# Performance work log

Hardware: AMD Instinct MI355X
Metric: run time of the kernel (lower is better)

Reference implementation:

```python
import jax, jax.numpy as jnp
import numpy as np

N_NODES = 50000
N_EDGES = 800000
IN_C = 32
HID = 64
N_LAYERS = 3
EDGE_HID = 128
OUT_C = 1
N_GRAPHS = 8


def setup_inputs() -> dict:
    key = jax.random.key(0)
    ks = jax.random.split(key, 32)
    x = jax.random.normal(ks[0], (N_NODES, IN_C), dtype=jnp.float32)
    # edges with src != dst so that PyG's remove_self_loops is a no-op
    src = jax.random.randint(ks[1], (N_EDGES,), 0, N_NODES)
    off = jax.random.randint(ks[2], (N_EDGES,), 1, N_NODES)
    dst = (src + off) % N_NODES
    edge_index = jnp.stack([src, dst]).astype(jnp.int32)
    batch = jnp.sort(jax.random.randint(ks[3], (N_NODES,), 0, N_GRAPHS)).astype(jnp.int32)
    inp = {"x": x, "edge_index": edge_index, "batch": batch}
    i = 4
    for l in range(N_LAYERS):
        din = IN_C if l == 0 else HID
        s = 1.0 / float(np.sqrt(din))
        inp[f"Wl{l}"] = jax.random.normal(ks[i], (din, HID), dtype=jnp.float32) * s; i += 1
        inp[f"bl{l}"] = jnp.zeros((HID,), jnp.float32)
        inp[f"Wr{l}"] = jax.random.normal(ks[i], (din, HID), dtype=jnp.float32) * s; i += 1
        inp[f"br{l}"] = jnp.zeros((HID,), jnp.float32)
        inp[f"att{l}"] = jax.random.normal(ks[i], (HID,), dtype=jnp.float32) * (1.0 / float(np.sqrt(HID))); i += 1
        inp[f"res{l}"] = jax.random.normal(ks[i], (din, HID), dtype=jnp.float32) * s; i += 1
        inp[f"bias{l}"] = jnp.zeros((HID,), jnp.float32)
        inp[f"lng{l}"] = jnp.ones((HID,), jnp.float32)
        inp[f"lnb{l}"] = jnp.zeros((HID,), jnp.float32)
    efd = 3 * HID
    inp["W1"] = jax.random.normal(ks[i], (efd, EDGE_HID), dtype=jnp.float32) * (1.0 / float(np.sqrt(efd))); i += 1
    inp["b1"] = jnp.zeros((EDGE_HID,), jnp.float32)
    inp["W2"] = jax.random.normal(ks[i], (EDGE_HID, OUT_C), dtype=jnp.float32) * (1.0 / float(np.sqrt(EDGE_HID))); i += 1
    inp["b2"] = jnp.zeros((OUT_C,), jnp.float32)
    return inp


def _gatv2_layer(x, src, dst, Wl, bl, Wr, br, att, resW, bias):
    # GATv2Conv (heads=1, share_weights=False, residual=True, add_self_loops handled by caller)
    n = x.shape[0]
    xl = x @ Wl + bl  # source transform  [N, C]
    xr = x @ Wr + br  # target transform  [N, C]
    e = jax.nn.leaky_relu(xl[src] + xr[dst], 0.2)  # [E, C]
    logits = e @ att                               # [E]
    m = jax.ops.segment_max(logits, dst, num_segments=n)
    ex = jnp.exp(logits - m[dst])
    denom = jax.ops.segment_sum(ex, dst, num_segments=n)
    alpha = ex / denom[dst]                        # edge softmax over incoming edges
    out = jax.ops.segment_sum(alpha[:, None] * xl[src], dst, num_segments=n)
    return out + x @ resW + bias


def _layernorm(h, g, b):
    mu = h.mean(-1, keepdims=True)
    var = h.var(-1, keepdims=True)
    return (h - mu) * jax.lax.rsqrt(var + 1e-5) * g + b


def reference(x, edge_index, batch,
              Wl0, bl0, Wr0, br0, att0, res0, bias0, lng0, lnb0,
              Wl1, bl1, Wr1, br1, att1, res1, bias1, lng1, lnb1,
              Wl2, bl2, Wr2, br2, att2, res2, bias2, lng2, lnb2,
              W1, b1, W2, b2):
    n = x.shape[0]
    loop = jnp.arange(n, dtype=edge_index.dtype)
    src = jnp.concatenate([edge_index[0], loop])  # add self loops
    dst = jnp.concatenate([edge_index[1], loop])
    layers = [(Wl0, bl0, Wr0, br0, att0, res0, bias0, lng0, lnb0),
              (Wl1, bl1, Wr1, br1, att1, res1, bias1, lng1, lnb1),
              (Wl2, bl2, Wr2, br2, att2, res2, bias2, lng2, lnb2)]
    h = x
    for (Wl, bl, Wr, br, att, resW, bias, g, b) in layers:
        h = _gatv2_layer(h, src, dst, Wl, bl, Wr, br, att, resW, bias)
        h = jax.nn.relu(_layernorm(h, g, b))
    node_repr = h
    gc = jax.ops.segment_sum(node_repr, batch, num_segments=N_GRAPHS)  # global_add_pool
    s, d = edge_index[0], edge_index[1]
    edge_feat = jnp.concatenate([node_repr[s], node_repr[d], gc[batch[s]]], axis=-1)  # [E, 3*HID]
    return jax.nn.relu(edge_feat @ W1 + b1) @ W2 + b2
```

## Files before the change

### kernel.cpp

```cpp
#include <hip/hip_runtime.h>
#include <math.h>

typedef float floatx2 __attribute__((ext_vector_type(2)));
typedef float floatx4 __attribute__((ext_vector_type(4)));
typedef short bf16x8 __attribute__((ext_vector_type(8)));
typedef _Float16 halfx2 __attribute__((ext_vector_type(2)));

#define NODE_MASK 0x07FFFFFF
#define LOG2E 1.4426950408889634f

__device__ __forceinline__ float wave_sum(float v){
#pragma unroll
  for (int m = 1; m < 64; m <<= 1) v += __shfl_xor(v, m, 64);
  return v;
}

__device__ __forceinline__ unsigned short bf16_of(float a){
  unsigned ua = __float_as_uint(a);
  ua = (ua + 0x7FFFu + ((ua >> 16) & 1u)) >> 16;
  return (unsigned short)ua;
}
__device__ __forceinline__ unsigned pack_bf16(float a, float b){
  unsigned ua = __float_as_uint(a), ub = __float_as_uint(b);
  ua = (ua + 0x7FFFu + ((ua >> 16) & 1u)) >> 16;
  ub = (ub + 0x7FFFu + ((ub >> 16) & 1u)) >> 16;
  return ua | (ub << 16);
}
__device__ __forceinline__ float2 unpack_bf16(unsigned p){
  float2 r;
  r.x = __uint_as_float(p << 16);
  r.y = __uint_as_float(p & 0xFFFF0000u);
  return r;
}
__device__ __forceinline__ bf16x8 to_bf16x8(float4 a, float4 b){
  bf16x8 r;
  r[0]=(short)bf16_of(a.x); r[1]=(short)bf16_of(a.y);
  r[2]=(short)bf16_of(a.z); r[3]=(short)bf16_of(a.w);
  r[4]=(short)bf16_of(b.x); r[5]=(short)bf16_of(b.y);
  r[6]=(short)bf16_of(b.z); r[7]=(short)bf16_of(b.w);
  return r;
}
__device__ __forceinline__ halfx2 f22h2(float a, float b){
  auto r = __builtin_amdgcn_cvt_pkrtz(a, b);
  return *(halfx2*)&r;
}
__device__ __forceinline__ float fdot2h(halfx2 a, halfx2 b, float c){
  return __builtin_amdgcn_fdot2(a, b, c, false);
}

__global__ void k_deg_rank(const int* __restrict__ dst, int* __restrict__ deg,
                           int* __restrict__ rank, int e){
  int i = (blockIdx.x*blockDim.x + threadIdx.x) * 4;
  if (i + 3 < e){
    int4 d4 = *(const int4*)&dst[i];
    int4 r4;
    r4.x = atomicAdd(&deg[d4.x], 1);
    r4.y = atomicAdd(&deg[d4.y], 1);
    r4.z = atomicAdd(&deg[d4.z], 1);
    r4.w = atomicAdd(&deg[d4.w], 1);
    *(int4*)&rank[i] = r4;
  } else {
    for (int j = i; j < e; ++j) rank[j] = atomicAdd(&deg[dst[j]], 1);
  }
}

__global__ void k_scan_a(const int* __restrict__ deg, int* __restrict__ rowptr,
                         int* __restrict__ bsum, int n){
  __shared__ int sm[256];
  int i = blockIdx.x*256 + threadIdx.x;
  int v = (i < n) ? (deg[i] + 1) : 0;
  sm[threadIdx.x] = v; __syncthreads();
#pragma unroll
  for (int off = 1; off < 256; off <<= 1){
    int t = (threadIdx.x >= off) ? sm[threadIdx.x - off] : 0;
    __syncthreads();
    sm[threadIdx.x] += t;
    __syncthreads();
  }
  if (i < n) rowptr[i] = sm[threadIdx.x] - v;
  if (threadIdx.x == 255) bsum[blockIdx.x] = sm[255];
}

__global__ void k_scan_b(int* __restrict__ bsum, int* __restrict__ rowptr, int nb, int n){
  __shared__ int sm[256];
  int t = threadIdx.x;
  int v = (t < nb) ? bsum[t] : 0;
  sm[t] = v; __syncthreads();
#pragma unroll
  for (int off = 1; off < 256; off <<= 1){
    int x = (t >= off) ? sm[t - off] : 0;
    __syncthreads();
    sm[t] += x;
    __syncthreads();
  }
  if (t < nb) bsum[t] = sm[t] - v;
  if (t == 255) rowptr[n] = sm[255];
}

__global__ void k_scan_c_selfloop(int* __restrict__ rowptr, const int* __restrict__ bsum,
                                  int* __restrict__ csr,
                                  const int* __restrict__ batch,
                                  float* __restrict__ gc, int n){
  int i = blockIdx.x*256 + threadIdx.x;
  if (i < n){
    int r = rowptr[i] + bsum[blockIdx.x];
    rowptr[i] = r;
    csr[r] = i | (batch[i] << 27);
  }
  if (blockIdx.x == 0){
    gc[threadIdx.x] = 0.f;
    gc[threadIdx.x + 256] = 0.f;
  }
}

__global__ void k_scatter(const int* __restrict__ src, const int* __restrict__ dst,
                          const int* __restrict__ batch,
                          const int* __restrict__ rowptr, const int* __restrict__ rank,
                          int* __restrict__ csr, int* __restrict__ epos, int e){
  int i = (blockIdx.x*blockDim.x + threadIdx.x) * 4;
  if (i + 3 < e){
    int4 s4 = *(const int4*)&src[i];
    int4 d4 = *(const int4*)&dst[i];
    int4 r4 = *(const int4*)&rank[i];
    int p0 = rowptr[d4.x] + 1 + r4.x;
    int p1 = rowptr[d4.y] + 1 + r4.y;
    int p2 = rowptr[d4.z] + 1 + r4.z;
    int p3 = rowptr[d4.w] + 1 + r4.w;
    csr[p0] = s4.x | (batch[s4.x] << 27);
    csr[p1] = s4.y | (batch[s4.y] << 27);
    csr[p2] = s4.z | (batch[s4.z] << 27);
    csr[p3] = s4.w | (batch[s4.w] << 27);
    int4 ep; ep.x = p0 - d4.x - 1; ep.y = p1 - d4.y - 1;
    ep.z = p2 - d4.z - 1; ep.w = p3 - d4.w - 1;
    *(int4*)&epos[i] = ep;
  } else {
    for (int j = i; j < e; ++j){
      int d = dst[j], sv = src[j];
      int pos = rowptr[d] + 1 + rank[j];
      csr[pos] = sv | (batch[sv] << 27);
      epos[j] = pos - d - 1;
    }
  }
}

template<int K>
__global__ __launch_bounds__(256)
void k_node_transform(const float* __restrict__ h,
                      const float* __restrict__ Wl, const float* __restrict__ bl,
                      const float* __restrict__ Wr, const float* __restrict__ br,
                      const float* __restrict__ Wres, const float* __restrict__ bias,
                      unsigned short* __restrict__ xl8, float* __restrict__ xr,
                      float* __restrict__ res, int n){
  const int KH = K / 32;
  int lane = threadIdx.x & 63;
  int nt   = threadIdx.x >> 6;
  int nn = lane & 15, q = lane >> 4;
  int m0 = blockIdx.x * 64;
  if (m0 >= n) return;
  bf16x8 Af[4][KH];
#pragma unroll
  for (int t = 0; t < 4; ++t){
#pragma unroll
    for (int kh = 0; kh < KH; ++kh){
      int node = min(m0 + t*16 + nn, n - 1);
      const float* hp = h + (size_t)node*K + kh*32 + q*8;
      Af[t][kh] = to_bf16x8(*(const float4*)hp, *(const float4*)(hp + 4));
    }
  }
  int n0 = nt * 16;
  for (int sel = 0; sel < 3; ++sel){
    const float* Wp = (sel == 0) ? Wl : (sel == 1) ? Wr : Wres;
    const float* bp = (sel == 0) ? bl : (sel == 1) ? br : bias;
    bf16x8 Bf[KH];
#pragma unroll
    for (int kh = 0; kh < KH; ++kh){
#pragma unroll
      for (int j = 0; j < 8; ++j)
        Bf[kh][j] = (short)bf16_of(Wp[(kh*32 + q*8 + j)*64 + n0 + nn]);
    }
    float bv = bp[n0 + nn];
#pragma unroll
    for (int t = 0; t < 4; ++t){
      floatx4 acc = {bv, bv, bv, bv};
#pragma unroll
      for (int kh = 0; kh < KH; ++kh)
        acc = __builtin_amdgcn_mfma_f32_16x16x32_bf16(Af[t][kh], Bf[kh], acc, 0, 0, 0);
      int nodeb = m0 + t*16 + q*4;
      if (sel == 0){
#pragma unroll
        for (int reg = 0; reg < 4; ++reg){
          float v = acc[reg];
          float p = __shfl_xor(v, 1, 64);
          int node = nodeb + reg;
          if (!(nn & 1) && node < n)
            xl8[(size_t)node*32 + ((n0 + nn) >> 1)] =
              (unsigned short)__builtin_amdgcn_cvt_pk_fp8_f32(v, p, 0, false);
        }
      } else {
        float* op = (sel == 1) ? xr : res;
#pragma unroll
        for (int reg = 0; reg < 4; ++reg){
          int node = nodeb + reg;
          if (node < n) op[(size_t)node*64 + n0 + nn] = acc[reg];
        }
      }
    }
  }
}

__global__ void k_gat_edge(const unsigned* __restrict__ xl_u, const float* __restrict__ xr,
                           const float* __restrict__ att,
                           const float* __restrict__ lng, const float* __restrict__ lnb,
                           const int* __restrict__ rowptr, const int* __restrict__ csr,
                           float* __restrict__ hio, int n){
  int node = (blockIdx.x*blockDim.x + threadIdx.x) >> 6;
  int lane = threadIdx.x & 63;
  if (node >= n) return;
  int sub = lane >> 4;
  int l   = lane & 15;
  size_t base = (size_t)node*64 + 4*l;
  float4 xrv  = *(const float4*)&xr[base];
  float4 attv = *(const float4*)&att[4*l];
  halfx2 xh0 = f22h2(xrv.x, xrv.y), xh1 = f22h2(xrv.z, xrv.w);
  halfx2 at0 = f22h2(attv.x*LOG2E, attv.y*LOG2E);
  halfx2 at1 = f22h2(attv.z*LOG2E, attv.w*LOG2E);
  halfx2 z2  = {(_Float16)0.f, (_Float16)0.f};
  halfx2 c02 = {(_Float16)0.2f, (_Float16)0.2f};
  int p0 = rowptr[node], p1 = rowptr[node+1];
  int deg = p1 - p0;
  int sreg = csr[p0 + min(lane, deg-1)];
  int rounds = (deg + 3) >> 2;
  float dsum = 0.f;
  float a0=0.f, a1=0.f, a2=0.f, a3=0.f;
  int e0 = sub;
  bool v0 = e0 < deg;
  int s0 = __shfl(sreg, v0 ? e0 : 0, 64) & NODE_MASK;
  unsigned x0 = xl_u[(size_t)s0*16 + l];
  int e1 = 4 + sub;
  bool v1 = e1 < deg;
  unsigned x1 = x0;
  if (rounds > 1){
    int s1;
    if (e1 < 64) s1 = __shfl(sreg, v1 ? e1 : 0, 64);
    else         s1 = csr[p0 + (v1 ? e1 : 0)];
    s1 &= NODE_MASK;
    x1 = xl_u[(size_t)s1*16 + l];
  }
  for (int r = 0; r < rounds; ++r){
    int en = 4*(r+2) + sub;
    bool vn = en < deg;
    unsigned xn = x0;
    if (r + 2 < rounds){
      int sn;
      if (en < 64) sn = __shfl(sreg, vn ? en : 0, 64);
      else         sn = csr[p0 + (vn ? en : 0)];
      sn &= NODE_MASK;
      xn = xl_u[(size_t)sn*16 + l];
    }
    floatx2 p01 = __builtin_amdgcn_cvt_pk_f32_fp8(x0, false);
    floatx2 p23 = __builtin_amdgcn_cvt_pk_f32_fp8(x0, true);
    halfx2 v0h = f22h2(p01.x, p01.y) + xh0;
    halfx2 v1h = f22h2(p23.x, p23.y) + xh1;
    halfx2 lr0 = __builtin_elementwise_min(v0h, z2) * c02 + __builtin_elementwise_max(v0h, z2);
    halfx2 lr1 = __builtin_elementwise_min(v1h, z2) * c02 + __builtin_elementwise_max(v1h, z2);
    float partial = fdot2h(lr1, at1, fdot2h(lr0, at0, 0.f));
#pragma unroll
    for (int mm = 1; mm < 16; mm <<= 1) partial += __shfl_xor(partial, mm, 64);
    float w = v0 ? exp2f(partial) : 0.f;
    dsum += w;
    a0 = fmaf(w, p01.x, a0);
    a1 = fmaf(w, p01.y, a1);
    a2 = fmaf(w, p23.x, a2);
    a3 = fmaf(w, p23.y, a3);
    x0 = x1; v0 = v1;
    x1 = xn; v1 = vn;
  }
#pragma unroll
  for (int off = 16; off < 64; off <<= 1){
    dsum += __shfl_xor(dsum, off, 64);
    a0 += __shfl_xor(a0, off, 64);
    a1 += __shfl_xor(a1, off, 64);
    a2 += __shfl_xor(a2, off, 64);
    a3 += __shfl_xor(a3, off, 64);
  }
  float4 resv = *(const float4*)&hio[base];
  float inv = __builtin_amdgcn_rcpf(dsum);
  float ox = fmaf(a0, inv, resv.x);
  float oy = fmaf(a1, inv, resv.y);
  float oz = fmaf(a2, inv, resv.z);
  float ow = fmaf(a3, inv, resv.w);
  float mean = wave_sum(ox + oy + oz + ow) * (1.f/256.f);
  float dx = ox - mean, dy = oy - mean, dz = oz - mean, dw = ow - mean;
  float var = wave_sum(fmaf(dx,dx, fmaf(dy,dy, fmaf(dz,dz, dw*dw)))) * (1.f/256.f);
  float rstd = rsqrtf(var + 1e-5f);
  if (sub == 0){
    float4 lg = *(const float4*)&lng[4*l];
    float4 lb = *(const float4*)&lnb[4*l];
    float4 out;
    out.x = fmaxf(fmaf(dx*rstd, lg.x, lb.x), 0.f);
    out.y = fmaxf(fmaf(dy*rstd, lg.y, lb.y), 0.f);
    out.z = fmaxf(fmaf(dz*rstd, lg.z, lb.z), 0.f);
    out.w = fmaxf(fmaf(dw*rstd, lg.w, lb.w), 0.f);
    *(float4*)&hio[base] = out;
  }
}

__global__ void k_pool(const float* __restrict__ h, const int* __restrict__ batch,
                       float* __restrict__ gc, int n){
  int wid  = (blockIdx.x*blockDim.x + threadIdx.x) >> 6;
  int lane = threadIdx.x & 63;
  int n0 = wid*64;
  if (n0 >= n) return;
  int n1 = min(n0+64, n);
  int curg = batch[n0];
  float s = 0.f;
  for (int i = n0; i < n1; ++i){
    int g = batch[i];
    if (g != curg){ atomicAdd(&gc[curg*64+lane], s); s = 0.f; curg = g; }
    s += h[(size_t)i*64 + lane];
  }
  atomicAdd(&gc[curg*64+lane], s);
}

__global__ void k_graph_proj(const float* __restrict__ gc, const float* __restrict__ W1,
                             const float* __restrict__ b1, unsigned* __restrict__ Gh){
  int g = threadIdx.x >> 7;
  int j = threadIdx.x & 127;
  float a = b1[j];
#pragma unroll 8
  for (int k = 0; k < 64; ++k) a = fmaf(gc[g*64+k], W1[(128+k)*128 + j], a);
  float p = __shfl_xor(a, 1, 64);
  if (!(j & 1)){
    halfx2 hv = f22h2(a, p);
    Gh[g*64 + (j >> 1)] = *(unsigned*)&hv;
  }
}

__global__ __launch_bounds__(256)
void k_node_proj(const float* __restrict__ nr, const float* __restrict__ W1,
                 unsigned short* __restrict__ Au16, unsigned* __restrict__ Bu, int n){
  int lane = threadIdx.x & 63;
  int wave = threadIdx.x >> 6;
  int nn = lane & 15, q = lane >> 4;
  int m0 = blockIdx.x * 64;
  if (m0 >= n) return;
  bf16x8 Af[4][2];
#pragma unroll
  for (int t = 0; t < 4; ++t){
#pragma unroll
    for (int kh = 0; kh < 2; ++kh){
      int node = min(m0 + t*16 + nn, n - 1);
      const float* hp = nr + (size_t)node*64 + kh*32 + q*8;
      Af[t][kh] = to_bf16x8(*(const float4*)hp, *(const float4*)(hp + 4));
    }
  }
  for (int half = 0; half < 2; ++half){
#pragma unroll
    for (int ni = 0; ni < 2; ++ni){
      int nt = wave + ni*4;
      int n0 = nt * 16;
      bf16x8 Bf[2];
#pragma unroll
      for (int kh = 0; kh < 2; ++kh){
#pragma unroll
        for (int j = 0; j < 8; ++j)
          Bf[kh][j] = (short)bf16_of(W1[(half*64 + kh*32 + q*8 + j)*128 + n0 + nn]);
      }
#pragma unroll
      for (int t = 0; t < 4; ++t){
        floatx4 acc = {0.f, 0.f, 0.f, 0.f};
#pragma unroll
        for (int kh = 0; kh < 2; ++kh)
          acc = __builtin_amdgcn_mfma_f32_16x16x32_bf16(Af[t][kh], Bf[kh], acc, 0, 0, 0);
        int nodeb = m0 + t*16 + q*4;
#pragma unroll
        for (int reg = 0; reg < 4; ++reg){
          float v = acc[reg];
          float p = __shfl_xor(v, 1, 64);
          int node = nodeb + reg;
          if (!(nn & 1) && node < n){
            int j = (n0 + nn) >> 1;
            if (half == 0)
              Au16[(size_t)node*64 + j] =
                (unsigned short)__builtin_amdgcn_cvt_pk_fp8_f32(v, p, 0, false);
            else
              Bu[(size_t)node*64 + j] = pack_bf16(v, p);
          }
        }
      }
    }
  }
}

__global__ void k_edge_out_csr(const uint2* __restrict__ Au2, const uint4* __restrict__ Bu4,
                               const unsigned* __restrict__ Gh,
                               const int* __restrict__ rowptr, const int* __restrict__ csr,
                               const float* __restrict__ W2, const float* __restrict__ b2,
                               float* __restrict__ tmp, int n){
  int node = (blockIdx.x*blockDim.x + threadIdx.x) >> 6;
  int lane = threadIdx.x & 63;
  if (node >= n) return;
  int sub = lane >> 4;
  int l   = lane & 15;
  int p0 = rowptr[node];
  int deg2 = rowptr[node+1] - p0 - 1;
  if (deg2 <= 0) return;
  int sreg = csr[p0 + 1 + min(lane, deg2-1)];
  uint4 b = Bu4[(size_t)node*16 + l];
  float2 b01 = unpack_bf16(b.x), b23 = unpack_bf16(b.y);
  float2 b45 = unpack_bf16(b.z), b67 = unpack_bf16(b.w);
  halfx2 bh0 = f22h2(b01.x, b01.y), bh1 = f22h2(b23.x, b23.y);
  halfx2 bh2 = f22h2(b45.x, b45.y), bh3 = f22h2(b67.x, b67.y);
  float4 w0 = *(const float4*)&W2[8*l];
  float4 w1 = *(const float4*)&W2[8*l + 4];
  halfx2 wh0 = f22h2(w0.x, w0.y), wh1 = f22h2(w0.z, w0.w);
  halfx2 wh2 = f22h2(w1.x, w1.y), wh3 = f22h2(w1.z, w1.w);
  halfx2 z2 = {(_Float16)0.f, (_Float16)0.f};
  float b2v = b2[0];
  int rbase = p0 - node;
  int rounds = (deg2 + 3) >> 2;
  int e0 = sub;
  bool v0 = e0 < deg2;
  int c0 = __shfl(sreg, v0 ? e0 : 0, 64);
  uint2 A0 = Au2[(size_t)(c0 & NODE_MASK)*16 + l];
  int e1 = 4 + sub;
  bool v1 = e1 < deg2;
  int c1 = c0; uint2 A1 = A0;
  if (rounds > 1){
    if (e1 < 64) c1 = __shfl(sreg, v1 ? e1 : 0, 64);
    else         c1 = csr[p0 + 1 + (v1 ? e1 : 0)];
    A1 = Au2[(size_t)(c1 & NODE_MASK)*16 + l];
  }
  for (int r = 0; r < rounds; ++r){
    int en = 4*(r+2) + sub;
    bool vn = en < deg2;
    int cn = c0; uint2 An = A0;
    if (r + 2 < rounds){
      if (en < 64) cn = __shfl(sreg, vn ? en : 0, 64);
      else         cn = csr[p0 + 1 + (vn ? en : 0)];
      An = Au2[(size_t)(cn & NODE_MASK)*16 + l];
    }
    int g = ((unsigned)c0) >> 27;
    uint4 gv = *(const uint4*)(Gh + g*64 + 4*l);
    halfx2 gh0 = *(halfx2*)&gv.x, gh1 = *(halfx2*)&gv.y;
    halfx2 gh2 = *(halfx2*)&gv.z, gh3 = *(halfx2*)&gv.w;
    floatx2 a01 = __builtin_amdgcn_cvt_pk_f32_fp8(A0.x, false);
    floatx2 a23 = __builtin_amdgcn_cvt_pk_f32_fp8(A0.x, true);
    floatx2 a45 = __builtin_amdgcn_cvt_pk_f32_fp8(A0.y, false);
    floatx2 a67 = __builtin_amdgcn_cvt_pk_f32_fp8(A0.y, true);
    halfx2 h0 = __builtin_elementwise_max(f22h2(a01.x, a01.y) + bh0 + gh0, z2);
    halfx2 h1 = __builtin_elementwise_max(f22h2(a23.x, a23.y) + bh1 + gh1, z2);
    halfx2 h2 = __builtin_elementwise_max(f22h2(a45.x, a45.y) + bh2 + gh2, z2);
    halfx2 h3 = __builtin_elementwise_max(f22h2(a67.x, a67.y) + bh3 + gh3, z2);
    float part = fdot2h(h3, wh3, fdot2h(h2, wh2, fdot2h(h1, wh1, fdot2h(h0, wh0, 0.f))));
#pragma unroll
    for (int mm = 1; mm < 16; mm <<= 1) part += __shfl_xor(part, mm, 64);
    if (l == 0 && v0) tmp[rbase + 4*r + sub] = part + b2v;
    c0 = c1; A0 = A1; v0 = v1;
    c1 = cn; A1 = An; v1 = vn;
  }
}

__global__ void k_remap(const float* __restrict__ tmp, const int* __restrict__ epos,
                        float* __restrict__ out, int e){
  int i = blockIdx.x*blockDim.x + threadIdx.x;
  if (i < e) out[i] = tmp[epos[i]];
}

extern "C" void kernel_launch(void* const* d_in, const int* in_sizes, int n_in,
                              void* d_out, int out_size, void* d_ws, size_t ws_size,
                              hipStream_t stream){
  const float* x     = (const float*)d_in[0];
  const int*   ei    = (const int*)d_in[1];
  const int*   batch = (const int*)d_in[2];
  const int N = in_sizes[2];
  const int E = in_sizes[1] / 2;
  const int* src = ei;
  const int* dst = ei + E;

  unsigned* W = (unsigned*)d_ws;
  const size_t N16 = (size_t)N * 16;
  const size_t N32 = (size_t)N * 32;
  const size_t N64 = (size_t)N * 64;
  unsigned short* xl8 = (unsigned short*)W;
  float* xr = (float*)(W + N16);
  float* hE = (float*)(W + N16 + N64);
  float* hD = (float*)(W + N16 + 2*N64);
  unsigned short* Au16 = (unsigned short*)W;
  unsigned* Bu = W + N32;
  int* rowptr = (int*)(W + N16 + 3*N64);
  int* deg    = rowptr + (N + 2);
  int* csr    = deg + N;
  int* epos   = csr + (N + E);
  int* rank   = epos + E;
  float* gc   = (float*)(rank + E);
  unsigned* Gh = (unsigned*)(gc + 512);
  int* bsum   = (int*)(Gh + 512);
  float* tmp  = (float*)(bsum + 256);

  const int NB = (N + 255) / 256;
  const int NT64 = (N + 63) / 64;

  (void)hipMemsetAsync(deg, 0, (size_t)N*4, stream);
  k_deg_rank <<<(E/4+255)/256, 256, 0, stream>>>(dst, deg, rank, E);
  k_scan_a   <<<NB, 256, 0, stream>>>(deg, rowptr, bsum, N);
  k_scan_b   <<<1, 256, 0, stream>>>(bsum, rowptr, NB, N);
  k_scan_c_selfloop<<<NB, 256, 0, stream>>>(rowptr, bsum, csr, batch, gc, N);
  k_scatter  <<<(E/4+255)/256, 256, 0, stream>>>(src, dst, batch, rowptr, rank, csr, epos, E);

  const float* h = x;
  float* hn = hD;
  for (int l = 0; l < 3; ++l){
    const float* Wl   = (const float*)d_in[3 + 9*l + 0];
    const float* bl   = (const float*)d_in[3 + 9*l + 1];
    const float* Wr   = (const float*)d_in[3 + 9*l + 2];
    const float* br   = (const float*)d_in[3 + 9*l + 3];
    const float* att  = (const float*)d_in[3 + 9*l + 4];
    const float* Wres = (const float*)d_in[3 + 9*l + 5];
    const float* bias = (const float*)d_in[3 + 9*l + 6];
    const float* lng  = (const float*)d_in[3 + 9*l + 7];
    const float* lnb  = (const float*)d_in[3 + 9*l + 8];
    if (l == 0)
      k_node_transform<32><<<NT64, 256, 0, stream>>>(h, Wl, bl, Wr, br, Wres, bias, xl8, xr, hn, N);
    else
      k_node_transform<64><<<NT64, 256, 0, stream>>>(h, Wl, bl, Wr, br, Wres, bias, xl8, xr, hn, N);
    k_gat_edge<<<(N+3)/4, 256, 0, stream>>>((const unsigned*)xl8, xr, att, lng, lnb, rowptr, csr, hn, N);
    h = hn;
    hn = (l == 0) ? hE : hD;
  }

  const float* W1 = (const float*)d_in[30];
  const float* b1 = (const float*)d_in[31];
  const float* W2 = (const float*)d_in[32];
  const float* b2 = (const float*)d_in[33];

  int pool_waves = (N + 63) / 64;
  k_pool      <<<(pool_waves+3)/4, 256, 0, stream>>>(hD, batch, gc, N);
  k_graph_proj<<<1, 1024, 0, stream>>>(gc, W1, b1, Gh);
  k_node_proj <<<NT64, 256, 0, stream>>>(hD, W1, Au16, Bu, N);
  k_edge_out_csr<<<(N+3)/4, 256, 0, stream>>>((const uint2*)Au16, (const uint4*)Bu, Gh,
                                              rowptr, csr, W2, b2, tmp, N);
  k_remap     <<<(E+255)/256, 256, 0, stream>>>(tmp, epos, (float*)d_out, E);
}
```

Before: 427.5 us.

## Process eight edges per wave round and scatter edge outputs directly

The GAT edge kernel and the edge-output kernel now map 8 lanes per edge and 8 edges per round instead of 16 lanes and 4 edges. Each lane loads wider vectors and the cross-lane reductions get shorter. The scatter kernel now records the original edge id at each CSR position, so the final kernel writes results straight to the output and the separate remap pass and temp buffer go away. In exchange, the output writes become scattered, and the edge kernel's second prefetch assumes index 8+sub is always below 64.

```diff
diff --git a/kernel.cpp b/kernel.cpp
--- a/kernel.cpp
+++ b/kernel.cpp
@@ -116,7 +116,7 @@
 __global__ void k_scatter(const int* __restrict__ src, const int* __restrict__ dst,
                           const int* __restrict__ batch,
                           const int* __restrict__ rowptr, const int* __restrict__ rank,
-                          int* __restrict__ csr, int* __restrict__ epos, int e){
+                          int* __restrict__ csr, int* __restrict__ eidA, int e){
   int i = (blockIdx.x*blockDim.x + threadIdx.x) * 4;
   if (i + 3 < e){
     int4 s4 = *(const int4*)&src[i];
@@ -130,15 +130,16 @@
     csr[p1] = s4.y | (batch[s4.y] << 27);
     csr[p2] = s4.z | (batch[s4.z] << 27);
     csr[p3] = s4.w | (batch[s4.w] << 27);
-    int4 ep; ep.x = p0 - d4.x - 1; ep.y = p1 - d4.y - 1;
-    ep.z = p2 - d4.z - 1; ep.w = p3 - d4.w - 1;
-    *(int4*)&epos[i] = ep;
+    eidA[p0] = i;
+    eidA[p1] = i + 1;
+    eidA[p2] = i + 2;
+    eidA[p3] = i + 3;
   } else {
     for (int j = i; j < e; ++j){
       int d = dst[j], sv = src[j];
       int pos = rowptr[d] + 1 + rank[j];
       csr[pos] = sv | (batch[sv] << 27);
-      epos[j] = pos - d - 1;
+      eidA[pos] = j;
     }
   }
 }
@@ -208,7 +209,7 @@
   }
 }
 
-__global__ void k_gat_edge(const unsigned* __restrict__ xl_u, const float* __restrict__ xr,
+__global__ void k_gat_edge(const uint2* __restrict__ xl_u2, const float* __restrict__ xr,
                            const float* __restrict__ att,
                            const float* __restrict__ lng, const float* __restrict__ lnb,
                            const int* __restrict__ rowptr, const int* __restrict__ csr,
@@ -216,92 +217,121 @@
   int node = (blockIdx.x*blockDim.x + threadIdx.x) >> 6;
   int lane = threadIdx.x & 63;
   if (node >= n) return;
-  int sub = lane >> 4;
-  int l   = lane & 15;
-  size_t base = (size_t)node*64 + 4*l;
-  float4 xrv  = *(const float4*)&xr[base];
-  float4 attv = *(const float4*)&att[4*l];
-  halfx2 xh0 = f22h2(xrv.x, xrv.y), xh1 = f22h2(xrv.z, xrv.w);
-  halfx2 at0 = f22h2(attv.x*LOG2E, attv.y*LOG2E);
-  halfx2 at1 = f22h2(attv.z*LOG2E, attv.w*LOG2E);
+  int sub = lane >> 3;
+  int l   = lane & 7;
+  size_t base = (size_t)node*64 + 8*l;
+  float4 xr0 = *(const float4*)&xr[base];
+  float4 xr1 = *(const float4*)&xr[base + 4];
+  float4 at0f = *(const float4*)&att[8*l];
+  float4 at1f = *(const float4*)&att[8*l + 4];
+  halfx2 xh0 = f22h2(xr0.x, xr0.y), xh1 = f22h2(xr0.z, xr0.w);
+  halfx2 xh2 = f22h2(xr1.x, xr1.y), xh3 = f22h2(xr1.z, xr1.w);
+  halfx2 at0 = f22h2(at0f.x*LOG2E, at0f.y*LOG2E);
+  halfx2 at1 = f22h2(at0f.z*LOG2E, at0f.w*LOG2E);
+  halfx2 at2 = f22h2(at1f.x*LOG2E, at1f.y*LOG2E);
+  halfx2 at3 = f22h2(at1f.z*LOG2E, at1f.w*LOG2E);
   halfx2 z2  = {(_Float16)0.f, (_Float16)0.f};
   halfx2 c02 = {(_Float16)0.2f, (_Float16)0.2f};
   int p0 = rowptr[node], p1 = rowptr[node+1];
   int deg = p1 - p0;
   int sreg = csr[p0 + min(lane, deg-1)];
-  int rounds = (deg + 3) >> 2;
+  int rounds = (deg + 7) >> 3;
   float dsum = 0.f;
-  float a0=0.f, a1=0.f, a2=0.f, a3=0.f;
+  float a0=0.f,a1=0.f,a2=0.f,a3=0.f,a4=0.f,a5=0.f,a6=0.f,a7=0.f;
   int e0 = sub;
   bool v0 = e0 < deg;
   int s0 = __shfl(sreg, v0 ? e0 : 0, 64) & NODE_MASK;
-  unsigned x0 = xl_u[(size_t)s0*16 + l];
-  int e1 = 4 + sub;
+  uint2 x0 = xl_u2[(size_t)s0*8 + l];
+  int e1 = 8 + sub;
   bool v1 = e1 < deg;
-  unsigned x1 = x0;
+  uint2 x1 = x0;
   if (rounds > 1){
-    int s1;
-    if (e1 < 64) s1 = __shfl(sreg, v1 ? e1 : 0, 64);
-    else         s1 = csr[p0 + (v1 ? e1 : 0)];
-    s1 &= NODE_MASK;
-    x1 = xl_u[(size_t)s1*16 + l];
+    int s1 = __shfl(sreg, v1 ? e1 : 0, 64) & NODE_MASK;
+    x1 = xl_u2[(size_t)s1*8 + l];
   }
   for (int r = 0; r < rounds; ++r){
-    int en = 4*(r+2) + sub;
+    int en = 8*(r+2) + sub;
     bool vn = en < deg;
-    unsigned xn = x0;
+    uint2 xn = x0;
     if (r + 2 < rounds){
       int sn;
       if (en < 64) sn = __shfl(sreg, vn ? en : 0, 64);
       else         sn = csr[p0 + (vn ? en : 0)];
       sn &= NODE_MASK;
-      xn = xl_u[(size_t)sn*16 + l];
-    }
-    floatx2 p01 = __builtin_amdgcn_cvt_pk_f32_fp8(x0, false);
-    floatx2 p23 = __builtin_amdgcn_cvt_pk_f32_fp8(x0, true);
+      xn = xl_u2[(size_t)sn*8 + l];
+    }
+    floatx2 p01 = __builtin_amdgcn_cvt_pk_f32_fp8(x0.x, false);
+    floatx2 p23 = __builtin_amdgcn_cvt_pk_f32_fp8(x0.x, true);
+    floatx2 p45 = __builtin_amdgcn_cvt_pk_f32_fp8(x0.y, false);
+    floatx2 p67 = __builtin_amdgcn_cvt_pk_f32_fp8(x0.y, true);
     halfx2 v0h = f22h2(p01.x, p01.y) + xh0;
     halfx2 v1h = f22h2(p23.x, p23.y) + xh1;
+    halfx2 v2h = f22h2(p45.x, p45.y) + xh2;
+    halfx2 v3h = f22h2(p67.x, p67.y) + xh3;
     halfx2 lr0 = __builtin_elementwise_min(v0h, z2) * c02 + __builtin_elementwise_max(v0h, z2);
     halfx2 lr1 = __builtin_elementwise_min(v1h, z2) * c02 + __builtin_elementwise_max(v1h, z2);
-    float partial = fdot2h(lr1, at1, fdot2h(lr0, at0, 0.f));
-#pragma unroll
-    for (int mm = 1; mm < 16; mm <<= 1) partial += __shfl_xor(partial, mm, 64);
+    halfx2 lr2 = __builtin_elementwise_min(v2h, z2) * c02 + __builtin_elementwise_max(v2h, z2);
+    halfx2 lr3 = __builtin_elementwise_min(v3h, z2) * c02 + __builtin_elementwise_max(v3h, z2);
+    float partial = fdot2h(lr3, at3, fdot2h(lr2, at2, fdot2h(lr1, at1, fdot2h(lr0, at0, 0.f))));
+#pragma unroll
+    for (int mm = 1; mm < 8; mm <<= 1) partial += __shfl_xor(partial, mm, 64);
     float w = v0 ? exp2f(partial) : 0.f;
     dsum += w;
     a0 = fmaf(w, p01.x, a0);
     a1 = fmaf(w, p01.y, a1);
     a2 = fmaf(w, p23.x, a2);
     a3 = fmaf(w, p23.y, a3);
+    a4 = fmaf(w, p45.x, a4);
+    a5 = fmaf(w, p45.y, a5);
+    a6 = fmaf(w, p67.x, a6);
+    a7 = fmaf(w, p67.y, a7);
     x0 = x1; v0 = v1;
     x1 = xn; v1 = vn;
   }
 #pragma unroll
-  for (int off = 16; off < 64; off <<= 1){
+  for (int off = 8; off < 64; off <<= 1){
     dsum += __shfl_xor(dsum, off, 64);
     a0 += __shfl_xor(a0, off, 64);
     a1 += __shfl_xor(a1, off, 64);
     a2 += __shfl_xor(a2, off, 64);
     a3 += __shfl_xor(a3, off, 64);
-  }
-  float4 resv = *(const float4*)&hio[base];
+    a4 += __shfl_xor(a4, off, 64);
+    a5 += __shfl_xor(a5, off, 64);
+    a6 += __shfl_xor(a6, off, 64);
+    a7 += __shfl_xor(a7, off, 64);
+  }
+  float4 r0 = *(const float4*)&hio[base];
+  float4 r1 = *(const float4*)&hio[base + 4];
   float inv = __builtin_amdgcn_rcpf(dsum);
-  float ox = fmaf(a0, inv, resv.x);
-  float oy = fmaf(a1, inv, resv.y);
-  float oz = fmaf(a2, inv, resv.z);
-  float ow = fmaf(a3, inv, resv.w);
-  float mean = wave_sum(ox + oy + oz + ow) * (1.f/256.f);
-  float dx = ox - mean, dy = oy - mean, dz = oz - mean, dw = ow - mean;
-  float var = wave_sum(fmaf(dx,dx, fmaf(dy,dy, fmaf(dz,dz, dw*dw)))) * (1.f/256.f);
+  float o0 = fmaf(a0, inv, r0.x);
+  float o1 = fmaf(a1, inv, r0.y);
+  float o2 = fmaf(a2, inv, r0.z);
+  float o3 = fmaf(a3, inv, r0.w);
+  float o4 = fmaf(a4, inv, r1.x);
+  float o5 = fmaf(a5, inv, r1.y);
+  float o6 = fmaf(a6, inv, r1.z);
+  float o7 = fmaf(a7, inv, r1.w);
+  float mean = wave_sum(o0+o1+o2+o3+o4+o5+o6+o7) * (1.f/512.f);
+  float d0 = o0-mean, d1 = o1-mean, d2 = o2-mean, d3 = o3-mean;
+  float d4 = o4-mean, d5 = o5-mean, d6 = o6-mean, d7 = o7-mean;
+  float var = wave_sum(d0*d0+d1*d1+d2*d2+d3*d3+d4*d4+d5*d5+d6*d6+d7*d7) * (1.f/512.f);
   float rstd = rsqrtf(var + 1e-5f);
   if (sub == 0){
-    float4 lg = *(const float4*)&lng[4*l];
-    float4 lb = *(const float4*)&lnb[4*l];
-    float4 out;
-    out.x = fmaxf(fmaf(dx*rstd, lg.x, lb.x), 0.f);
-    out.y = fmaxf(fmaf(dy*rstd, lg.y, lb.y), 0.f);
-    out.z = fmaxf(fmaf(dz*rstd, lg.z, lb.z), 0.f);
-    out.w = fmaxf(fmaf(dw*rstd, lg.w, lb.w), 0.f);
-    *(float4*)&hio[base] = out;
+    float4 lg0 = *(const float4*)&lng[8*l];
+    float4 lg1 = *(const float4*)&lng[8*l + 4];
+    float4 lb0 = *(const float4*)&lnb[8*l];
+    float4 lb1 = *(const float4*)&lnb[8*l + 4];
+    float4 out0, out1;
+    out0.x = fmaxf(fmaf(d0*rstd, lg0.x, lb0.x), 0.f);
+    out0.y = fmaxf(fmaf(d1*rstd, lg0.y, lb0.y), 0.f);
+    out0.z = fmaxf(fmaf(d2*rstd, lg0.z, lb0.z), 0.f);
+    out0.w = fmaxf(fmaf(d3*rstd, lg0.w, lb0.w), 0.f);
+    out1.x = fmaxf(fmaf(d4*rstd, lg1.x, lb1.x), 0.f);
+    out1.y = fmaxf(fmaf(d5*rstd, lg1.y, lb1.y), 0.f);
+    out1.z = fmaxf(fmaf(d6*rstd, lg1.z, lb1.z), 0.f);
+    out1.w = fmaxf(fmaf(d7*rstd, lg1.w, lb1.w), 0.f);
+    *(float4*)&hio[base] = out0;
+    *(float4*)&hio[base + 4] = out1;
   }
 }
 
@@ -392,79 +422,100 @@
   }
 }
 
-__global__ void k_edge_out_csr(const uint2* __restrict__ Au2, const uint4* __restrict__ Bu4,
+__global__ void k_edge_out_csr(const uint4* __restrict__ Au4, const uint4* __restrict__ Bu4,
                                const unsigned* __restrict__ Gh,
                                const int* __restrict__ rowptr, const int* __restrict__ csr,
+                               const int* __restrict__ eidA,
                                const float* __restrict__ W2, const float* __restrict__ b2,
-                               float* __restrict__ tmp, int n){
+                               float* __restrict__ out, int n){
   int node = (blockIdx.x*blockDim.x + threadIdx.x) >> 6;
   int lane = threadIdx.x & 63;
   if (node >= n) return;
-  int sub = lane >> 4;
-  int l   = lane & 15;
+  int sub = lane >> 3;
+  int l   = lane & 7;
   int p0 = rowptr[node];
   int deg2 = rowptr[node+1] - p0 - 1;
   if (deg2 <= 0) return;
-  int sreg = csr[p0 + 1 + min(lane, deg2-1)];
-  uint4 b = Bu4[(size_t)node*16 + l];
-  float2 b01 = unpack_bf16(b.x), b23 = unpack_bf16(b.y);
-  float2 b45 = unpack_bf16(b.z), b67 = unpack_bf16(b.w);
-  halfx2 bh0 = f22h2(b01.x, b01.y), bh1 = f22h2(b23.x, b23.y);
-  halfx2 bh2 = f22h2(b45.x, b45.y), bh3 = f22h2(b67.x, b67.y);
-  float4 w0 = *(const float4*)&W2[8*l];
-  float4 w1 = *(const float4*)&W2[8*l + 4];
+  int idx = p0 + 1 + min(lane, deg2-1);
+  int sreg = csr[idx];
+  int ereg = eidA[idx];
+  uint4 ba = Bu4[(size_t)node*16 + 2*l];
+  uint4 bb = Bu4[(size_t)node*16 + 2*l + 1];
+  float2 t0 = unpack_bf16(ba.x), t1 = unpack_bf16(ba.y);
+  float2 t2 = unpack_bf16(ba.z), t3 = unpack_bf16(ba.w);
+  float2 t4 = unpack_bf16(bb.x), t5 = unpack_bf16(bb.y);
+  float2 t6 = unpack_bf16(bb.z), t7 = unpack_bf16(bb.w);
+  halfx2 bh0 = f22h2(t0.x, t0.y), bh1 = f22h2(t1.x, t1.y);
+  halfx2 bh2 = f22h2(t2.x, t2.y), bh3 = f22h2(t3.x, t3.y);
+  halfx2 bh4 = f22h2(t4.x, t4.y), bh5 = f22h2(t5.x, t5.y);
+  halfx2 bh6 = f22h2(t6.x, t6.y), bh7 = f22h2(t7.x, t7.y);
+  float4 w0 = *(const float4*)&W2[16*l];
+  float4 w1 = *(const float4*)&W2[16*l + 4];
+  float4 w2 = *(const float4*)&W2[16*l + 8];
+  float4 w3 = *(const float4*)&W2[16*l + 12];
   halfx2 wh0 = f22h2(w0.x, w0.y), wh1 = f22h2(w0.z, w0.w);
   halfx2 wh2 = f22h2(w1.x, w1.y), wh3 = f22h2(w1.z, w1.w);
+  halfx2 wh4 = f22h2(w2.x, w2.y), wh5 = f22h2(w2.z, w2.w);
+  halfx2 wh6 = f22h2(w3.x, w3.y), wh7 = f22h2(w3.z, w3.w);
   halfx2 z2 = {(_Float16)0.f, (_Float16)0.f};
   float b2v = b2[0];
-  int rbase = p0 - node;
-  int rounds = (deg2 + 3) >> 2;
+  int rounds = (deg2 + 7) >> 3;
   int e0 = sub;
   bool v0 = e0 < deg2;
-  int c0 = __shfl(sreg, v0 ? e0 : 0, 64);
-  uint2 A0 = Au2[(size_t)(c0 & NODE_MASK)*16 + l];
-  int e1 = 4 + sub;
+  int q0 = v0 ? e0 : 0;
+  int c0 = __shfl(sreg, q0, 64);
+  int id0 = __shfl(ereg, q0, 64);
+  uint4 A0 = Au4[(size_t)(c0 & NODE_MASK)*8 + l];
+  int e1 = 8 + sub;
   bool v1 = e1 < deg2;
-  int c1 = c0; uint2 A1 = A0;
+  int c1 = c0, id1 = id0; uint4 A1 = A0;
   if (rounds > 1){
-    if (e1 < 64) c1 = __shfl(sreg, v1 ? e1 : 0, 64);
-    else         c1 = csr[p0 + 1 + (v1 ? e1 : 0)];
-    A1 = Au2[(size_t)(c1 & NODE_MASK)*16 + l];
+    int q1 = v1 ? e1 : 0;
+    c1 = __shfl(sreg, q1, 64);
+    id1 = __shfl(ereg, q1, 64);
+    A1 = Au4[(size_t)(c1 & NODE_MASK)*8 + l];
   }
   for (int r = 0; r < rounds; ++r){
-    int en = 4*(r+2) + sub;
+    int en = 8*(r+2) + sub;
     bool vn = en < deg2;
-    int cn = c0; uint2 An = A0;
+    int cn = c0, idn = id0; uint4 An = A0;
     if (r + 2 < rounds){
-      if (en < 64) cn = __shfl(sreg, vn ? en : 0, 64);
-      else         cn = csr[p0 + 1 + (vn ? en : 0)];
-      An = Au2[(size_t)(cn & NODE_MASK)*16 + l];
+      int qn = vn ? en : 0;
+      if (en < 64){ cn = __shfl(sreg, qn, 64); idn = __shfl(ereg, qn, 64); }
+      else        { cn = csr[p0 + 1 + qn];     idn = eidA[p0 + 1 + qn]; }
+      An = Au4[(size_t)(cn & NODE_MASK)*8 + l];
     }
     int g = ((unsigned)c0) >> 27;
-    uint4 gv = *(const uint4*)(Gh + g*64 + 4*l);
-    halfx2 gh0 = *(halfx2*)&gv.x, gh1 = *(halfx2*)&gv.y;
-    halfx2 gh2 = *(halfx2*)&gv.z, gh3 = *(halfx2*)&gv.w;
+    const uint4* gp = (const uint4*)(Gh + g*64 + 8*l);
+    uint4 g0 = gp[0], g1 = gp[1];
+    halfx2 gh0 = *(halfx2*)&g0.x, gh1 = *(halfx2*)&g0.y;
+    halfx2 gh2 = *(halfx2*)&g0.z, gh3 = *(halfx2*)&g0.w;
+    halfx2 gh4 = *(halfx2*)&g1.x, gh5 = *(halfx2*)&g1.y;
+    halfx2 gh6 = *(halfx2*)&g1.z, gh7 = *(halfx2*)&g1.w;
     floatx2 a01 = __builtin_amdgcn_cvt_pk_f32_fp8(A0.x, false);
     floatx2 a23 = __builtin_amdgcn_cvt_pk_f32_fp8(A0.x, true);
     floatx2 a45 = __builtin_amdgcn_cvt_pk_f32_fp8(A0.y, false);
     floatx2 a67 = __builtin_amdgcn_cvt_pk_f32_fp8(A0.y, true);
+    floatx2 a89 = __builtin_amdgcn_cvt_pk_f32_fp8(A0.z, false);
+    floatx2 aab = __builtin_amdgcn_cvt_pk_f32_fp8(A0.z, true);
+    floatx2 acd = __builtin_amdgcn_cvt_pk_f32_fp8(A0.w, false);
+    floatx2 aef = __builtin_amdgcn_cvt_pk_f32_fp8(A0.w, true);
     halfx2 h0 = __builtin_elementwise_max(f22h2(a01.x, a01.y) + bh0 + gh0, z2);
     halfx2 h1 = __builtin_elementwise_max(f22h2(a23.x, a23.y) + bh1 + gh1, z2);
     halfx2 h2 = __builtin_elementwise_max(f22h2(a45.x, a45.y) + bh2 + gh2, z2);
     halfx2 h3 = __builtin_elementwise_max(f22h2(a67.x, a67.y) + bh3 + gh3, z2);
-    float part = fdot2h(h3, wh3, fdot2h(h2, wh2, fdot2h(h1, wh1, fdot2h(h0, wh0, 0.f))));
-#pragma unroll
-    for (int mm = 1; mm < 16; mm <<= 1) part += __shfl_xor(part, mm, 64);
-    if (l == 0 && v0) tmp[rbase + 4*r + sub] = part + b2v;
-    c0 = c1; A0 = A1; v0 = v1;
-    c1 = cn; A1 = An; v1 = vn;
-  }
-}
-
-__global__ void k_remap(const float* __restrict__ tmp, const int* __restrict__ epos,
-                        float* __restrict__ out, int e){
-  int i = blockIdx.x*blockDim.x + threadIdx.x;
-  if (i < e) out[i] = tmp[epos[i]];
+    halfx2 h4 = __builtin_elementwise_max(f22h2(a89.x, a89.y) + bh4 + gh4, z2);
+    halfx2 h5 = __builtin_elementwise_max(f22h2(aab.x, aab.y) + bh5 + gh5, z2);
+    halfx2 h6 = __builtin_elementwise_max(f22h2(acd.x, acd.y) + bh6 + gh6, z2);
+    halfx2 h7 = __builtin_elementwise_max(f22h2(aef.x, aef.y) + bh7 + gh7, z2);
+    float part = fdot2h(h7, wh7, fdot2h(h6, wh6, fdot2h(h5, wh5, fdot2h(h4, wh4,
+                 fdot2h(h3, wh3, fdot2h(h2, wh2, fdot2h(h1, wh1, fdot2h(h0, wh0, 0.f))))))));
+#pragma unroll
+    for (int mm = 1; mm < 8; mm <<= 1) part += __shfl_xor(part, mm, 64);
+    if (l == 0 && v0) out[id0] = part + b2v;
+    c0 = c1; id0 = id1; A0 = A1; v0 = v1;
+    c1 = cn; id1 = idn; A1 = An; v1 = vn;
+  }
 }
 
 extern "C" void kernel_launch(void* const* d_in, const int* in_sizes, int n_in,
@@ -489,14 +540,13 @@
   unsigned short* Au16 = (unsigned short*)W;
   unsigned* Bu = W + N32;
   int* rowptr = (int*)(W + N16 + 3*N64);
-  int* deg    = rowptr + (N + 2);
+  int* deg    = rowptr + (N + 16);
   int* csr    = deg + N;
-  int* epos   = csr + (N + E);
-  int* rank   = epos + E;
-  float* gc   = (float*)(rank + E);
+  int* rank   = csr + (N + E);
+  int* eidA   = rank + E;
+  float* gc   = (float*)(eidA + (N + E));
   unsigned* Gh = (unsigned*)(gc + 512);
   int* bsum   = (int*)(Gh + 512);
-  float* tmp  = (float*)(bsum + 256);
 
   const int NB = (N + 255) / 256;
   const int NT64 = (N + 63) / 64;
@@ -506,7 +556,7 @@
   k_scan_a   <<<NB, 256, 0, stream>>>(deg, rowptr, bsum, N);
   k_scan_b   <<<1, 256, 0, stream>>>(bsum, rowptr, NB, N);
   k_scan_c_selfloop<<<NB, 256, 0, stream>>>(rowptr, bsum, csr, batch, gc, N);
-  k_scatter  <<<(E/4+255)/256, 256, 0, stream>>>(src, dst, batch, rowptr, rank, csr, epos, E);
+  k_scatter  <<<(E/4+255)/256, 256, 0, stream>>>(src, dst, batch, rowptr, rank, csr, eidA, E);
 
   const float* h = x;
   float* hn = hD;
@@ -524,7 +574,7 @@
       k_node_transform<32><<<NT64, 256, 0, stream>>>(h, Wl, bl, Wr, br, Wres, bias, xl8, xr, hn, N);
     else
       k_node_transform<64><<<NT64, 256, 0, stream>>>(h, Wl, bl, Wr, br, Wres, bias, xl8, xr, hn, N);
-    k_gat_edge<<<(N+3)/4, 256, 0, stream>>>((const unsigned*)xl8, xr, att, lng, lnb, rowptr, csr, hn, N);
+    k_gat_edge<<<(N+3)/4, 256, 0, stream>>>((const uint2*)xl8, xr, att, lng, lnb, rowptr, csr, hn, N);
     h = hn;
     hn = (l == 0) ? hE : hD;
   }
@@ -538,7 +588,6 @@
   k_pool      <<<(pool_waves+3)/4, 256, 0, stream>>>(hD, batch, gc, N);
   k_graph_proj<<<1, 1024, 0, stream>>>(gc, W1, b1, Gh);
   k_node_proj <<<NT64, 256, 0, stream>>>(hD, W1, Au16, Bu, N);
-  k_edge_out_csr<<<(N+3)/4, 256, 0, stream>>>((const uint2*)Au16, (const uint4*)Bu, Gh,
-                                              rowptr, csr, W2, b2, tmp, N);
-  k_remap     <<<(E+255)/256, 256, 0, stream>>>(tmp, epos, (float*)d_out, E);
-}
+  k_edge_out_csr<<<(N+3)/4, 256, 0, stream>>>((const uint4*)Au16, (const uint4*)Bu, Gh,
+                                              rowptr, csr, eidA, W2, b2, (float*)d_out, N);
+}
```

Measured after the change: 421.2 us. Within noise of the previous version (-1.5%).
